# Performance work log

Measured on AMD Instinct MI355X. Metric: run time of the kernel, lower is better.

## Reference

```python
import jax, jax.numpy as jnp
import numpy as np

B, ROI, DIN = 1024, 200, 200
ENDS = [41, 70, 91, 110, 130, 137, 158, 200]
STARTS = [0] + ENDS[:-1]
NSUB = len(ENDS)
SEG = np.concatenate([np.full(e - s, i) for i, (s, e) in enumerate(zip(STARTS, ENDS))])  # [ROI]
COUNTS = np.array(ENDS) - np.array(STARTS)
MEAN_MAT = np.zeros((NSUB, ROI), dtype=np.float32)
MEAN_MAT[SEG, np.arange(ROI)] = 1.0 / COUNTS[SEG]
EPS = 1e-5


def _leaky(x):
    return jax.nn.leaky_relu(x, 0.2)


def _bn2d(x, g, b):
    # torch BatchNorm1d (training): biased var over batch dim
    m = x.mean(0)
    v = x.var(0)
    return (x - m) * jax.lax.rsqrt(v + EPS) * g + b


def _bn3d(x, g, b):
    # x: [B, C, L]; stats over (B, L) per channel
    m = x.mean(axis=(0, 2), keepdims=True)
    v = x.var(axis=(0, 2), keepdims=True)
    return (x - m) * jax.lax.rsqrt(v + EPS) * g[None, :, None] + b[None, :, None]


def _block(x, rs_intra, rs_inter, mean_mat, seg):
    # einsum 'ijk,ijp->ijp' == row-sum scaling
    intra = rs_intra * x                                   # [B,R,F]
    sub = jnp.einsum('sr,brf->bsf', mean_mat, x)           # segment means [B,8,F]
    sub = rs_inter * sub                                   # inter row-sum scaling
    prop = sub[:, seg, :]                                  # broadcast back to nodes
    return (intra + prop) * 0.5


def setup_inputs() -> dict:
    key = jax.random.key(0)
    ks = jax.random.split(key, 24)
    s = 0.05
    d = {
        'adjacency_matrix': jax.random.uniform(ks[0], (B, ROI, ROI), jnp.float32),
        'intra_adjacency': jax.random.uniform(ks[1], (B, ROI, ROI), jnp.float32),
        'inter_adjacency': jax.random.uniform(ks[2], (B, NSUB, NSUB), jnp.float32),
        'node_features': jax.random.normal(ks[3], (B, ROI, DIN), jnp.float32),
        'W0': jax.random.normal(ks[4], (DIN, ROI)) * s, 'b0': jnp.zeros((ROI,)),
        'W1': jax.random.normal(ks[5], (ROI, ROI)) * s, 'b1': jnp.zeros((ROI,)),
        'g1': jnp.ones((ROI,)), 'be1': jnp.zeros((ROI,)),
        'W2': jax.random.normal(ks[6], (ROI, ROI)) * s, 'b2': jnp.zeros((ROI,)),
        'g2': jnp.ones((ROI,)), 'be2': jnp.zeros((ROI,)),
        'W3': jax.random.normal(ks[7], (ROI, 64)) * s, 'b3': jnp.zeros((64,)),
        'W4': jax.random.normal(ks[8], (64, 8)) * s, 'b4': jnp.zeros((8,)),
        'g3': jnp.ones((ROI,)), 'be3': jnp.zeros((ROI,)),
        'Wc1': jax.random.normal(ks[9], (8 * ROI, 256)) * s, 'bc1': jnp.zeros((256,)),
        'Wc2': jax.random.normal(ks[10], (256, 32)) * s, 'bc2': jnp.zeros((32,)),
        'Wc3': jax.random.normal(ks[11], (32, 2)) * s, 'bc3': jnp.zeros((2,)),
    }
    return d


def reference(adjacency_matrix, intra_adjacency, inter_adjacency, node_features,
              W0, b0, W1, b1, g1, be1, W2, b2, g2, be2,
              W3, b3, W4, b4, g3, be3, Wc1, bc1, Wc2, bc2, Wc3, bc3):
    mean_mat = jnp.asarray(MEAN_MAT)
    seg = jnp.asarray(SEG)
    rs_intra = intra_adjacency.sum(-1, keepdims=True)   # [B,R,1]
    rs_inter = inter_adjacency.sum(-1, keepdims=True)   # [B,8,1]

    x = _block(node_features, rs_intra, rs_inter, mean_mat, seg)
    x = _leaky(x @ W0 + b0) @ W1 + b1                    # gcn -> [B,R,ROI]
    x = _bn2d(x.reshape(B * ROI, ROI), g1, be1).reshape(B, ROI, ROI)

    x = _block(x, rs_intra, rs_inter, mean_mat, seg)
    x = _leaky(x @ W2 + b2)                              # gcn1
    x = _bn2d(x.reshape(B * ROI, ROI), g2, be2).reshape(B, ROI, ROI)

    x = _block(x, rs_intra, rs_inter, mean_mat, seg)
    x = _leaky(_leaky(x @ W3 + b3) @ W4 + b4)            # gcn2 -> [B,R,8]
    x = _bn3d(x, g3, be3)

    x = x.reshape(B, 8 * ROI)
    x = _leaky(x @ Wc1 + bc1)
    x = _leaky(x @ Wc2 + bc2)
    return x @ Wc3 + bc3
```

## Files before the change

### kernel.cpp

```cpp
#include <hip/hip_runtime.h>
#include <hip/hip_bf16.h>

#define BDIM 1024
#define ROI 200
#define DIN 200
#define NSUB 8
#define NROWS (BDIM * ROI)
#define XELEMS ((size_t)NROWS * 200)
#define PLPAD 32
#define PLSZ (XELEMS + PLPAD)

typedef __attribute__((ext_vector_type(8))) short short8;
typedef __attribute__((ext_vector_type(4))) float f32x4;

__device__ __constant__ float d_invcnt[8] = {
    1.f/41.f, 1.f/29.f, 1.f/21.f, 1.f/19.f, 1.f/20.f, 1.f/7.f, 1.f/21.f, 1.f/42.f};

__device__ inline unsigned short f2bf_rn(float x) {
  unsigned u = __float_as_uint(x);
  return (unsigned short)((u + 0x7FFFu + ((u >> 16) & 1u)) >> 16);
}
__device__ constexpr int seg_of_c(int r) {
  return (r < 41) ? 0 : (r < 70) ? 1 : (r < 91) ? 2 : (r < 110) ? 3
       : (r < 130) ? 4 : (r < 137) ? 5 : (r < 158) ? 6 : 7;
}

__device__ inline void gload_lds16(const unsigned short* src, unsigned short* dst) {
  __builtin_amdgcn_global_load_lds(
      (const __attribute__((address_space(1))) void*)src,
      (__attribute__((address_space(3))) void*)dst, 16, 0, 0);
}

__global__ __launch_bounds__(256) void rowint_k(const float* __restrict__ intra,
                                                const float* __restrict__ inter,
                                                float* __restrict__ rsI,
                                                float* __restrict__ rsP) {
  if (blockIdx.x < NROWS / 4) {
    int row = blockIdx.x * 4 + (threadIdx.x >> 6);
    int lane = threadIdx.x & 63;
    const float* p = intra + (size_t)row * 200;
    float v = p[lane] + p[lane + 64] + p[lane + 128];
    if (lane < 8) v += p[lane + 192];
    #pragma unroll
    for (int off = 32; off > 0; off >>= 1) v += __shfl_down(v, off);
    if (lane == 0) rsI[row] = v;
  } else {
    int i = (blockIdx.x - NROWS / 4) * 256 + threadIdx.x;
    if (i < BDIM * NSUB) {
      const float* p = inter + (size_t)i * 8;
      float v = 0.f;
      #pragma unroll
      for (int c = 0; c < 8; ++c) v += p[c];
      rsP[i] = v;
    }
  }
}

__global__ __launch_bounds__(128) void seg_combine_f32_k(
    const float* __restrict__ xf, const float* __restrict__ rsI,
    const float* __restrict__ rsP, unsigned short* __restrict__ yp) {
  int b = blockIdx.x;
  int t = threadIdx.x;
  if (t >= 100) return;
  int c0 = 2 * t;
  size_t base = (size_t)b * 40000 + c0;
  float a0[8] = {0,0,0,0,0,0,0,0};
  float a1[8] = {0,0,0,0,0,0,0,0};
  #pragma unroll
  for (int r = 0; r < 200; ++r) {
    float2 fv = *(const float2*)(xf + base + (size_t)r * 200);
    int s = seg_of_c(r);
    a0[s] += fv.x; a1[s] += fv.y;
  }
  float pr0[8], pr1[8];
  #pragma unroll
  for (int s = 0; s < 8; ++s) {
    float rp = rsP[b * 8 + s];
    pr0[s] = rp * a0[s] * d_invcnt[s];
    pr1[s] = rp * a1[s] * d_invcnt[s];
  }
  const float* rsIb = rsI + b * 200;
  #pragma unroll
  for (int r = 0; r < 200; ++r) {
    size_t idx = base + (size_t)r * 200;
    float2 fv = *(const float2*)(xf + idx);
    int s = seg_of_c(r);
    float ri = rsIb[r];
    float y0 = 0.5f * (ri * fv.x + pr0[s]);
    float y1 = 0.5f * (ri * fv.y + pr1[s]);
    *(unsigned*)(yp + idx) = (unsigned)f2bf_rn(y0) | ((unsigned)f2bf_rn(y1) << 16);
  }
}

__global__ __launch_bounds__(128) void seg_combine_bn_k(
    const unsigned short* __restrict__ xp, const float* __restrict__ rsI,
    const float* __restrict__ rsP, const float* __restrict__ stats,
    const float* __restrict__ g, const float* __restrict__ be,
    unsigned short* __restrict__ yp) {
  const float invN = 1.f / (float)NROWS;
  int b = blockIdx.x;
  int t = threadIdx.x;
  if (t >= 100) return;
  int c0 = 2 * t;
  float m0 = stats[c0] * invN;
  float va0 = stats[200 + c0] * invN - m0 * m0;
  float sc0 = rsqrtf(va0 + 1e-5f) * g[c0];
  float sh0 = be[c0] - m0 * sc0;
  float m1 = stats[c0 + 1] * invN;
  float va1 = stats[200 + c0 + 1] * invN - m1 * m1;
  float sc1 = rsqrtf(va1 + 1e-5f) * g[c0 + 1];
  float sh1 = be[c0 + 1] - m1 * sc1;
  size_t base = (size_t)b * 40000 + c0;
  float a0[8] = {0,0,0,0,0,0,0,0};
  float a1[8] = {0,0,0,0,0,0,0,0};
  #pragma unroll
  for (int r = 0; r < 200; ++r) {
    unsigned u = *(const unsigned*)(xp + base + (size_t)r * 200);
    int s = seg_of_c(r);
    a0[s] += __uint_as_float(u << 16);
    a1[s] += __uint_as_float(u & 0xFFFF0000u);
  }
  float pr0[8], pr1[8];
  #pragma unroll
  for (int s = 0; s < 8; ++s) {
    float mm0 = a0[s] * d_invcnt[s] * sc0 + sh0;
    float mm1 = a1[s] * d_invcnt[s] * sc1 + sh1;
    float rp = rsP[b * 8 + s];
    pr0[s] = rp * mm0; pr1[s] = rp * mm1;
  }
  const float* rsIb = rsI + b * 200;
  #pragma unroll
  for (int r = 0; r < 200; ++r) {
    size_t idx = base + (size_t)r * 200;
    unsigned u = *(const unsigned*)(xp + idx);
    float v0 = __uint_as_float(u << 16) * sc0 + sh0;
    float v1 = __uint_as_float(u & 0xFFFF0000u) * sc1 + sh1;
    int s = seg_of_c(r);
    float ri = rsIb[r];
    float y0 = 0.5f * (ri * v0 + pr0[s]);
    float y1 = 0.5f * (ri * v1 + pr1[s]);
    *(unsigned*)(yp + idx) = (unsigned)f2bf_rn(y0) | ((unsigned)f2bf_rn(y1) << 16);
  }
}

__device__ inline void wconv_one(const float* __restrict__ W, int K, int N,
                                 int NFRAG, int KSTEPS, int idx,
                                 unsigned short* __restrict__ dst) {
  int j = idx & 7;
  int lane = (idx >> 3) & 63;
  int rest = idx >> 9;
  int frag = rest % NFRAG;
  int rest2 = rest / NFRAG;
  int ks = rest2 % KSTEPS;
  int cb = rest2 / KSTEPS;
  int k = ks * 32 + ((lane >> 4) << 3) + j;
  int col = cb * NFRAG * 16 + frag * 16 + (lane & 15);
  float v = (k < K && col < N) ? W[(size_t)k * N + col] : 0.f;
  dst[idx] = f2bf_rn(v);
}

__global__ __launch_bounds__(256) void wconv_all_k(
    const float* __restrict__ W0, const float* __restrict__ W1,
    const float* __restrict__ W2, const float* __restrict__ W3,
    const float* __restrict__ W4,
    unsigned short* __restrict__ w0f, unsigned short* __restrict__ w1f,
    unsigned short* __restrict__ w2f, unsigned short* __restrict__ w3f,
    unsigned short* __restrict__ w4f) {
  const int R = 50176;
  const int R3 = 14336;
  const int R4 = 1024;
  int id = blockIdx.x * 256 + threadIdx.x;
  if (id < R)                    wconv_one(W0, 200, 200, 7, 7, id, w0f);
  else if (id < 2 * R)           wconv_one(W1, 200, 200, 7, 7, id - R, w1f);
  else if (id < 3 * R)           wconv_one(W2, 200, 200, 7, 7, id - 2 * R, w2f);
  else if (id < 3 * R + R3)      wconv_one(W3, 200, 64, 4, 7, id - 3 * R, w3f);
  else if (id < 3 * R + R3 + R4) wconv_one(W4, 64, 8, 1, 2, id - 3 * R - R3, w4f);
}

template<int ACT, int STATS>
__global__ __launch_bounds__(512, 1) void gemm_bf3_k(
    const unsigned short* __restrict__ A, const unsigned short* __restrict__ Wf,
    const float* __restrict__ bias, unsigned short* __restrict__ Cp,
    float* __restrict__ stats) {
  constexpr int G = 7 * 7 * 64;
  __shared__ unsigned short wlds[G * 8];
  __shared__ unsigned short abuf[8][2][400 * 8];
  __shared__ float s_sum[112];
  __shared__ float s_sq[112];
  int tid = threadIdx.x;
  int lane = tid & 63;
  int wid = tid >> 6;
  int cb = blockIdx.y;

  const unsigned short* wsrc = Wf + (size_t)cb * G * 8;
  for (int g0 = wid * 64; g0 < G; g0 += 512)
    gload_lds16(wsrc + (size_t)(g0 + lane) * 8, &wlds[(size_t)g0 * 8]);
  if (STATS && tid < 112) { s_sum[tid] = 0.f; s_sq[tid] = 0.f; }

  int gw = blockIdx.x * 8 + wid;
  const int stride = 1024, nt = 12800;
  int row = lane & 15;
  int laneg = lane >> 4;

  auto issue_tile = [&](int t, unsigned short* buf) {
    const unsigned short* src = A + (size_t)t * 3200;
    #pragma unroll
    for (int j = 0; j < 7; ++j) {
      int slot = j * 64 + lane;
      if (slot < 400)
        gload_lds16(src + (size_t)slot * 8, buf + (size_t)j * 512);
    }
  };

  issue_tile(gw, &abuf[wid][0][0]);
  issue_tile(gw + stride, &abuf[wid][1][0]);
  __syncthreads();

  float lsum[7], lsq[7];
  #pragma unroll
  for (int f = 0; f < 7; ++f) { lsum[f] = 0.f; lsq[f] = 0.f; }
  int colbase = cb * 112;

  for (int i = 0; ; ++i) {
    int t = gw + i * stride;
    if (t >= nt) break;
    if (i) {
      asm volatile("s_waitcnt vmcnt(47)" ::: "memory");
      __builtin_amdgcn_sched_barrier(0);
    }
    const unsigned short* ab = &abuf[wid][i & 1][0];
    short8 av[7];
    #pragma unroll
    for (int ks = 0; ks < 7; ++ks) {
      int cs = ks * 4 + laneg;
      if (cs > 24) cs = 0;
      av[ks] = *(const short8*)&ab[(size_t)(row * 25 + cs) * 8];
    }
    asm volatile("s_waitcnt lgkmcnt(0)" ::: "memory");
    __builtin_amdgcn_sched_barrier(0);
    {
      int t2 = t + 2 * stride;
      issue_tile(t2 < nt ? t2 : gw, &abuf[wid][i & 1][0]);
    }
    __builtin_amdgcn_sched_barrier(0);
    f32x4 acc[7];
    #pragma unroll
    for (int f = 0; f < 7; ++f) acc[f] = 0.0f;
    #pragma unroll
    for (int ks = 0; ks < 7; ++ks) {
      const short8* wp = (const short8*)wlds + (size_t)(ks * 7) * 64 + lane;
      #pragma unroll
      for (int f = 0; f < 7; ++f) {
        short8 wv = wp[(size_t)f * 64];
        acc[f] = __builtin_amdgcn_mfma_f32_16x16x32_bf16(av[ks], wv, acc[f], 0, 0, 0);
      }
    }
    int row0 = t * 16 + laneg * 4;
    #pragma unroll
    for (int f = 0; f < 7; ++f) {
      int col = colbase + f * 16 + row;
      if (col < 200) {
        float b = bias[col];
        #pragma unroll
        for (int r = 0; r < 4; ++r) {
          float v = acc[f][r] + b;
          if (ACT) v = (v >= 0.f) ? v : 0.2f * v;
          Cp[(size_t)(row0 + r) * 200 + col] = f2bf_rn(v);
          if (STATS) { lsum[f] += v; lsq[f] += v * v; }
        }
      }
    }
    __builtin_amdgcn_sched_barrier(0);
  }

  if (STATS) {
    #pragma unroll
    for (int f = 0; f < 7; ++f) {
      float s = lsum[f] + __shfl_xor(lsum[f], 16);
      s += __shfl_xor(s, 32);
      float q = lsq[f] + __shfl_xor(lsq[f], 16);
      q += __shfl_xor(q, 32);
      if (laneg == 0) {
        atomicAdd(&s_sum[f * 16 + row], s);
        atomicAdd(&s_sq[f * 16 + row], q);
      }
    }
    __syncthreads();
    if (tid < 112) {
      int col = colbase + tid;
      if (col < 200) {
        atomicAdd(&stats[col], s_sum[tid]);
        atomicAdd(&stats[200 + col], s_sq[tid]);
      }
    }
  }
}

__global__ __launch_bounds__(512, 1) void gemm_w34s_k(
    const unsigned short* __restrict__ A, const unsigned short* __restrict__ W3f,
    const unsigned short* __restrict__ W4f, const float* __restrict__ b3,
    const float* __restrict__ b4, unsigned short* __restrict__ xcls) {
  __shared__ unsigned short w3lds[1792 * 8];
  __shared__ unsigned short w4lds[128 * 8];
  __shared__ unsigned short abuf[8][2][400 * 8];
  __shared__ unsigned short h3buf[8][16][72];
  int tid = threadIdx.x;
  int lane = tid & 63;
  int wid = tid >> 6;

  for (int g0 = wid * 64; g0 < 1792; g0 += 512)
    gload_lds16(W3f + (size_t)(g0 + lane) * 8, &w3lds[(size_t)g0 * 8]);
  if (wid == 0)
    for (int g0 = 0; g0 < 128; g0 += 64)
      gload_lds16(W4f + (size_t)(g0 + lane) * 8, &w4lds[(size_t)g0 * 8]);

  int gw = blockIdx.x * 8 + wid;
  const int stride = 1024, nt = 12800;
  int row = lane & 15;
  int laneg = lane >> 4;

  auto issue_tile = [&](int t, unsigned short* buf) {
    const unsigned short* src = A + (size_t)t * 3200;
    #pragma unroll
    for (int j = 0; j < 7; ++j) {
      int slot = j * 64 + lane;
      if (slot < 400)
        gload_lds16(src + (size_t)slot * 8, buf + (size_t)j * 512);
    }
  };

  issue_tile(gw, &abuf[wid][0][0]);
  issue_tile(gw + stride, &abuf[wid][1][0]);
  __syncthreads();

  for (int i = 0; ; ++i) {
    int t = gw + i * stride;
    if (t >= nt) break;
    if (i) {
      asm volatile("s_waitcnt vmcnt(15)" ::: "memory");
      __builtin_amdgcn_sched_barrier(0);
    }
    const unsigned short* ab = &abuf[wid][i & 1][0];
    short8 av[7];
    #pragma unroll
    for (int ks = 0; ks < 7; ++ks) {
      int cs = ks * 4 + laneg;
      if (cs > 24) cs = 0;
      av[ks] = *(const short8*)&ab[(size_t)(row * 25 + cs) * 8];
    }
    asm volatile("s_waitcnt lgkmcnt(0)" ::: "memory");
    __builtin_amdgcn_sched_barrier(0);
    {
      int t2 = t + 2 * stride;
      issue_tile(t2 < nt ? t2 : gw, &abuf[wid][i & 1][0]);
    }
    __builtin_amdgcn_sched_barrier(0);
    f32x4 acc[4];
    #pragma unroll
    for (int f = 0; f < 4; ++f) acc[f] = 0.0f;
    #pragma unroll
    for (int ks = 0; ks < 7; ++ks) {
      const short8* wp = (const short8*)w3lds + (size_t)(ks * 4) * 64 + lane;
      #pragma unroll
      for (int f = 0; f < 4; ++f) {
        short8 wv = wp[(size_t)f * 64];
        acc[f] = __builtin_amdgcn_mfma_f32_16x16x32_bf16(av[ks], wv, acc[f], 0, 0, 0);
      }
    }
    int r0 = laneg * 4;
    #pragma unroll
    for (int f = 0; f < 4; ++f) {
      int col = f * 16 + row;
      float bb = b3[col];
      #pragma unroll
      for (int r = 0; r < 4; ++r) {
        float v = acc[f][r] + bb;
        v = (v >= 0.f) ? v : 0.2f * v;
        h3buf[wid][r0 + r][col] = f2bf_rn(v);
      }
    }
    f32x4 acc2 = 0.0f;
    #pragma unroll
    for (int ks = 0; ks < 2; ++ks) {
      short8 a2 = *(const short8*)&h3buf[wid][row][ks * 32 + laneg * 8];
      short8 wv = *(const short8*)&w4lds[(size_t)(ks * 64 + lane) * 8];
      acc2 = __builtin_amdgcn_mfma_f32_16x16x32_bf16(a2, wv, acc2, 0, 0, 0);
    }
    int col = lane & 15;
    if (col < 8) {
      float bb = b4[col];
      #pragma unroll
      for (int r = 0; r < 4; ++r) {
        int rr = t * 16 + r0 + r;
        float v = acc2[r] + bb;
        v = (v >= 0.f) ? v : 0.2f * v;
        xcls[(size_t)(rr / 200) * 1600 + (rr % 200) * 8 + col] = f2bf_rn(v);
      }
    }
    __builtin_amdgcn_sched_barrier(0);
  }
}

__global__ __launch_bounds__(256) void bn3d_stats_bf_k(const unsigned short* __restrict__ x,
                                                       float* __restrict__ stats) {
  int t = threadIdx.x;
  if (t >= 200) return;
  const unsigned short* p = x + (size_t)blockIdx.x * 16 * 1600 + t * 8;
  float s = 0.f, q = 0.f;
  for (int b = 0; b < 16; ++b) {
    const unsigned* u = (const unsigned*)(p + (size_t)b * 1600);
    #pragma unroll
    for (int i = 0; i < 4; ++i) {
      unsigned w = u[i];
      float v0 = __uint_as_float(w << 16);
      float v1 = __uint_as_float(w & 0xFFFF0000u);
      s += v0 + v1;
      q += v0 * v0 + v1 * v1;
    }
  }
  atomicAdd(&stats[t], s);
  atomicAdd(&stats[200 + t], q);
}

__global__ __launch_bounds__(256) void wcls_conv_k(const float* __restrict__ Wc1,
                                                   const float* __restrict__ stats,
                                                   const float* __restrict__ g3,
                                                   unsigned short* __restrict__ dst) {
  const float invN = 1.f / 8192.f;
  int idx = blockIdx.x * 256 + threadIdx.x;
  if (idx >= 409600) return;
  int j = idx & 7;
  int lane = (idx >> 3) & 63;
  int rest = idx >> 9;
  int frag = rest & 3;
  int rest2 = rest >> 2;
  int ks = rest2 % 10;
  int slice = rest2 / 10;
  int kc = slice % 5, cb = slice / 5;
  int k = kc * 320 + ks * 32 + ((lane >> 4) << 3) + j;
  int col = cb * 64 + frag * 16 + (lane & 15);
  int r = k >> 3;
  float m = stats[r] * invN;
  float var = stats[200 + r] * invN - m * m;
  float scv = rsqrtf(var + 1e-5f) * g3[r];
  dst[idx] = f2bf_rn(Wc1[(size_t)k * 256 + col] * scv);
}

__global__ __launch_bounds__(256) void bias1_acc_k(const float* __restrict__ Wc1,
                                                   const float* __restrict__ stats,
                                                   const float* __restrict__ g3,
                                                   const float* __restrict__ be3,
                                                   float* __restrict__ bias1p) {
  const float invN = 1.f / 8192.f;
  int t = threadIdx.x;
  int k0 = blockIdx.x * 100;
  float a = 0.f;
  #pragma unroll 4
  for (int k = k0; k < k0 + 100; ++k) {
    int r = k >> 3;
    float m = stats[r] * invN;
    float var = stats[200 + r] * invN - m * m;
    float scv = rsqrtf(var + 1e-5f) * g3[r];
    float sh = be3[r] - m * scv;
    a += sh * Wc1[(size_t)k * 256 + t];
  }
  atomicAdd(&bias1p[t], a);
}

__global__ __launch_bounds__(256, 3) void gemm_cls1_k(
    const unsigned short* __restrict__ xcls, const unsigned short* __restrict__ Wf,
    float* __restrict__ h1f) {
  __shared__ unsigned short wlds[10 * 4 * 64 * 8];
  int tid = threadIdx.x;
  int lane = tid & 63;
  int wid = tid >> 6;
  const unsigned short* wsrc = Wf + (size_t)(blockIdx.y * 5 + blockIdx.z) * (10 * 4 * 64) * 8;
  for (int g0 = wid * 64; g0 < 2560; g0 += 256)
    gload_lds16(wsrc + (size_t)(g0 + lane) * 8, &wlds[(size_t)g0 * 8]);

  int row0 = blockIdx.x * 128 + wid * 32;
  int kbase = blockIdx.z * 320;
  const unsigned short* pA = xcls + (size_t)(row0 + (lane & 15)) * 1600 + kbase + ((lane >> 4) << 3);
  const unsigned short* pB = pA + 16 * 1600;
  short8 aA[10], aB[10];
  #pragma unroll
  for (int i = 0; i < 10; ++i) {
    aA[i] = *(const short8*)(pA + i * 32);
    aB[i] = *(const short8*)(pB + i * 32);
  }
  __builtin_amdgcn_sched_barrier(0);
  __syncthreads();

  f32x4 accA[4], accB[4];
  #pragma unroll
  for (int f = 0; f < 4; ++f) { accA[f] = 0.0f; accB[f] = 0.0f; }
  #pragma unroll
  for (int ks = 0; ks < 10; ++ks) {
    const short8* wp = (const short8*)wlds + (size_t)(ks * 4) * 64 + lane;
    #pragma unroll
    for (int f = 0; f < 4; ++f) {
      short8 wv = wp[(size_t)f * 64];
      accA[f] = __builtin_amdgcn_mfma_f32_16x16x32_bf16(aA[ks], wv, accA[f], 0, 0, 0);
      accB[f] = __builtin_amdgcn_mfma_f32_16x16x32_bf16(aB[ks], wv, accB[f], 0, 0, 0);
    }
  }
  int colbase = blockIdx.y * 64;
  int r0 = (lane >> 4) * 4;
  #pragma unroll
  for (int f = 0; f < 4; ++f) {
    int col = colbase + f * 16 + (lane & 15);
    #pragma unroll
    for (int r = 0; r < 4; ++r) {
      atomicAdd(&h1f[(size_t)(row0 + r0 + r) * 256 + col], accA[f][r]);
      atomicAdd(&h1f[(size_t)(row0 + 16 + r0 + r) * 256 + col], accB[f][r]);
    }
  }
}

__global__ __launch_bounds__(256) void classifier2_k(
    const float* __restrict__ h1f, const float* __restrict__ bias1p,
    const float* __restrict__ bc1,
    const float* __restrict__ Wc2, const float* __restrict__ bc2,
    const float* __restrict__ Wc3, const float* __restrict__ bc3,
    float* __restrict__ out) {
  __shared__ float h1s[8][256];
  __shared__ float h2s[8][32];
  int t = threadIdx.x;
  int b0 = blockIdx.x * 8;
  float bsum = bias1p[t] + bc1[t];
  #pragma unroll
  for (int j = 0; j < 8; ++j) {
    float v = h1f[(size_t)(b0 + j) * 256 + t] + bsum;
    h1s[j][t] = (v >= 0.f) ? v : 0.2f * v;
  }
  __syncthreads();
  {
    int j = t >> 5, c = t & 31;
    float a = 0.f;
    #pragma unroll 8
    for (int k = 0; k < 256; ++k) a += h1s[j][k] * Wc2[k * 32 + c];
    float v = a + bc2[c];
    h2s[j][c] = (v >= 0.f) ? v : 0.2f * v;
  }
  __syncthreads();
  if (t < 16) {
    int j = t >> 1, c = t & 1;
    float a = 0.f;
    #pragma unroll
    for (int k = 0; k < 32; ++k) a += h2s[j][k] * Wc3[k * 2 + c];
    out[(size_t)(b0 + j) * 2 + c] = a + bc3[c];
  }
}

extern "C" void kernel_launch(void* const* d_in, const int* in_sizes, int n_in,
                              void* d_out, int out_size, void* d_ws, size_t ws_size,
                              hipStream_t stream) {
  const float* intra = (const float*)d_in[1];
  const float* inter = (const float*)d_in[2];
  const float* nodef = (const float*)d_in[3];
  const float* W0 = (const float*)d_in[4];
  const float* b0 = (const float*)d_in[5];
  const float* W1 = (const float*)d_in[6];
  const float* b1 = (const float*)d_in[7];
  const float* g1 = (const float*)d_in[8];
  const float* be1 = (const float*)d_in[9];
  const float* W2 = (const float*)d_in[10];
  const float* b2 = (const float*)d_in[11];
  const float* g2 = (const float*)d_in[12];
  const float* be2 = (const float*)d_in[13];
  const float* W3 = (const float*)d_in[14];
  const float* b3 = (const float*)d_in[15];
  const float* W4 = (const float*)d_in[16];
  const float* b4 = (const float*)d_in[17];
  const float* g3 = (const float*)d_in[18];
  const float* be3 = (const float*)d_in[19];
  const float* Wc1 = (const float*)d_in[20];
  const float* bc1 = (const float*)d_in[21];
  const float* Wc2 = (const float*)d_in[22];
  const float* bc2 = (const float*)d_in[23];
  const float* Wc3 = (const float*)d_in[24];
  const float* bc3 = (const float*)d_in[25];
  float* out = (float*)d_out;

  unsigned short* P0 = (unsigned short*)d_ws;
  unsigned short* P1 = P0 + PLSZ;
  float* fbase = (float*)(P1 + PLSZ);
  float* rsI   = fbase;
  float* rsP   = rsI + NROWS;
  float* statsA = rsP + BDIM * 8;
  float* stats0 = statsA;
  float* stats1 = statsA + 512;
  float* stats2 = statsA + 1024;
  float* bias1p = statsA + 2048;
  float* h1f    = bias1p + 512;
  unsigned short* wt = (unsigned short*)(h1f + (size_t)BDIM * 256);
  const size_t W200SZ = 2 * 7 * 7 * 64 * 8;
  const size_t W3SZ   = 1 * 7 * 4 * 64 * 8;
  const size_t W4SZ   = 1 * 2 * 1 * 64 * 8;
  unsigned short* w0f = wt;
  unsigned short* w1f = w0f + W200SZ;
  unsigned short* w2f = w1f + W200SZ;
  unsigned short* w3f = w2f + W200SZ;
  unsigned short* w4f = w3f + W3SZ;
  unsigned short* wc1f = w4f + W4SZ;
  unsigned short* xcls = P0;

  hipMemsetAsync(statsA, 0, (2048 + 512 + (size_t)BDIM * 256) * sizeof(float), stream);

  wconv_all_k<<<648, 256, 0, stream>>>(W0, W1, W2, W3, W4, w0f, w1f, w2f, w3f, w4f);

  rowint_k<<<NROWS / 4 + 32, 256, 0, stream>>>(intra, inter, rsI, rsP);

  seg_combine_f32_k<<<BDIM, 128, 0, stream>>>(nodef, rsI, rsP, P0);

  gemm_bf3_k<1, 0><<<dim3(128, 2), 512, 0, stream>>>(P0, w0f, b0, P1, nullptr);
  gemm_bf3_k<0, 1><<<dim3(128, 2), 512, 0, stream>>>(P1, w1f, b1, P0, stats0);

  seg_combine_bn_k<<<BDIM, 128, 0, stream>>>(P0, rsI, rsP, stats0, g1, be1, P1);

  gemm_bf3_k<1, 1><<<dim3(128, 2), 512, 0, stream>>>(P1, w2f, b2, P0, stats1);

  seg_combine_bn_k<<<BDIM, 128, 0, stream>>>(P0, rsI, rsP, stats1, g2, be2, P1);

  gemm_w34s_k<<<128, 512, 0, stream>>>(P1, w3f, w4f, b3, b4, xcls);

  bn3d_stats_bf_k<<<64, 256, 0, stream>>>(xcls, stats2);
  wcls_conv_k<<<1600, 256, 0, stream>>>(Wc1, stats2, g3, wc1f);
  bias1_acc_k<<<16, 256, 0, stream>>>(Wc1, stats2, g3, be3, bias1p);

  gemm_cls1_k<<<dim3(8, 4, 5), 256, 0, stream>>>(xcls, wc1f, h1f);
  classifier2_k<<<BDIM / 8, 256, 0, stream>>>(h1f, bias1p, bc1, Wc2, bc2, Wc3, bc3, out);
}
```

Before: 407.6 us.

## Hold GEMM weight fragments in registers and split output columns across wave groups

```diff
diff --git a/kernel.cpp b/kernel.cpp
--- a/kernel.cpp
+++ b/kernel.cpp
@@ -178,12 +178,10 @@
 }
 
 template<int ACT, int STATS>
-__global__ __launch_bounds__(512, 1) void gemm_bf3_k(
+__global__ __launch_bounds__(512, 1) void gemm_bf4_k(
     const unsigned short* __restrict__ A, const unsigned short* __restrict__ Wf,
     const float* __restrict__ bias, unsigned short* __restrict__ Cp,
     float* __restrict__ stats) {
-  constexpr int G = 7 * 7 * 64;
-  __shared__ unsigned short wlds[G * 8];
   __shared__ unsigned short abuf[8][2][400 * 8];
   __shared__ float s_sum[112];
   __shared__ float s_sq[112];
@@ -191,14 +189,25 @@
   int lane = tid & 63;
   int wid = tid >> 6;
   int cb = blockIdx.y;
-
-  const unsigned short* wsrc = Wf + (size_t)cb * G * 8;
-  for (int g0 = wid * 64; g0 < G; g0 += 512)
-    gload_lds16(wsrc + (size_t)(g0 + lane) * 8, &wlds[(size_t)g0 * 8]);
+  int pid = wid & 3;
+  int grp = wid >> 2;
+  int f0 = grp * 4;
+
+  const unsigned short* wsrc = Wf + (size_t)cb * (49 * 64) * 8;
+  short8 wreg[28];
+  #pragma unroll
+  for (int ks = 0; ks < 7; ++ks) {
+    #pragma unroll
+    for (int f = 0; f < 4; ++f) {
+      int fe = f0 + f;
+      int fa = fe < 7 ? fe : 6;
+      wreg[ks * 4 + f] = *(const short8*)&wsrc[(size_t)((ks * 7 + fa) * 64 + lane) * 8];
+    }
+  }
   if (STATS && tid < 112) { s_sum[tid] = 0.f; s_sq[tid] = 0.f; }
 
-  int gw = blockIdx.x * 8 + wid;
-  const int stride = 1024, nt = 12800;
+  int gw = blockIdx.x * 4 + pid;
+  const int stride = 512, nt = 12800;
   int row = lane & 15;
   int laneg = lane >> 4;
 
@@ -216,16 +225,16 @@
   issue_tile(gw + stride, &abuf[wid][1][0]);
   __syncthreads();
 
-  float lsum[7], lsq[7];
-  #pragma unroll
-  for (int f = 0; f < 7; ++f) { lsum[f] = 0.f; lsq[f] = 0.f; }
+  float lsum[4], lsq[4];
+  #pragma unroll
+  for (int f = 0; f < 4; ++f) { lsum[f] = 0.f; lsq[f] = 0.f; }
   int colbase = cb * 112;
 
   for (int i = 0; ; ++i) {
     int t = gw + i * stride;
     if (t >= nt) break;
     if (i) {
-      asm volatile("s_waitcnt vmcnt(47)" ::: "memory");
+      asm volatile("s_waitcnt vmcnt(7)" ::: "memory");
       __builtin_amdgcn_sched_barrier(0);
     }
     const unsigned short* ab = &abuf[wid][i & 1][0];
@@ -243,23 +252,22 @@
       issue_tile(t2 < nt ? t2 : gw, &abuf[wid][i & 1][0]);
     }
     __builtin_amdgcn_sched_barrier(0);
-    f32x4 acc[7];
-    #pragma unroll
-    for (int f = 0; f < 7; ++f) acc[f] = 0.0f;
+    f32x4 acc[4];
+    #pragma unroll
+    for (int f = 0; f < 4; ++f) acc[f] = 0.0f;
     #pragma unroll
     for (int ks = 0; ks < 7; ++ks) {
-      const short8* wp = (const short8*)wlds + (size_t)(ks * 7) * 64 + lane;
       #pragma unroll
-      for (int f = 0; f < 7; ++f) {
-        short8 wv = wp[(size_t)f * 64];
-        acc[f] = __builtin_amdgcn_mfma_f32_16x16x32_bf16(av[ks], wv, acc[f], 0, 0, 0);
+      for (int f = 0; f < 4; ++f) {
+        acc[f] = __builtin_amdgcn_mfma_f32_16x16x32_bf16(av[ks], wreg[ks * 4 + f], acc[f], 0, 0, 0);
       }
     }
     int row0 = t * 16 + laneg * 4;
     #pragma unroll
-    for (int f = 0; f < 7; ++f) {
-      int col = colbase + f * 16 + row;
-      if (col < 200) {
+    for (int f = 0; f < 4; ++f) {
+      int fe = f0 + f;
+      int col = colbase + fe * 16 + row;
+      if (fe < 7 && col < 200) {
         float b = bias[col];
         #pragma unroll
         for (int r = 0; r < 4; ++r) {
@@ -275,14 +283,15 @@
 
   if (STATS) {
     #pragma unroll
-    for (int f = 0; f < 7; ++f) {
+    for (int f = 0; f < 4; ++f) {
+      int fe = f0 + f;
       float s = lsum[f] + __shfl_xor(lsum[f], 16);
       s += __shfl_xor(s, 32);
       float q = lsq[f] + __shfl_xor(lsq[f], 16);
       q += __shfl_xor(q, 32);
-      if (laneg == 0) {
-        atomicAdd(&s_sum[f * 16 + row], s);
-        atomicAdd(&s_sq[f * 16 + row], q);
+      if (laneg == 0 && fe < 7) {
+        atomicAdd(&s_sum[fe * 16 + row], s);
+        atomicAdd(&s_sq[fe * 16 + row], q);
       }
     }
     __syncthreads();
@@ -613,12 +622,12 @@
 
   seg_combine_f32_k<<<BDIM, 128, 0, stream>>>(nodef, rsI, rsP, P0);
 
-  gemm_bf3_k<1, 0><<<dim3(128, 2), 512, 0, stream>>>(P0, w0f, b0, P1, nullptr);
-  gemm_bf3_k<0, 1><<<dim3(128, 2), 512, 0, stream>>>(P1, w1f, b1, P0, stats0);
+  gemm_bf4_k<1, 0><<<dim3(128, 2), 512, 0, stream>>>(P0, w0f, b0, P1, nullptr);
+  gemm_bf4_k<0, 1><<<dim3(128, 2), 512, 0, stream>>>(P1, w1f, b1, P0, stats0);
 
   seg_combine_bn_k<<<BDIM, 128, 0, stream>>>(P0, rsI, rsP, stats0, g1, be1, P1);
 
-  gemm_bf3_k<1, 1><<<dim3(128, 2), 512, 0, stream>>>(P1, w2f, b2, P0, stats1);
+  gemm_bf4_k<1, 1><<<dim3(128, 2), 512, 0, stream>>>(P1, w2f, b2, P0, stats1);
 
   seg_combine_bn_k<<<BDIM, 128, 0, stream>>>(P0, rsI, rsP, stats1, g2, be2, P1);
 
```

Result: slower. 422.0 us (+3.5%).
